# Kernel tuning notes

Hardware: AMD Instinct MI355X
Metric: run time of the kernel (lower is better)

The kernel has to match this reference:

```python
import jax, jax.numpy as jnp
import numpy as np

N_MODES = 4
N_STAGES = 7
CTRL_HIDDEN = 128
PASS_DIM = 32
MAX_PASSES = 12


def _ln(x, g, b, eps=1e-5):
    m = x.mean(-1, keepdims=True)
    v = ((x - m) ** 2).mean(-1, keepdims=True)
    return (x - m) * jax.lax.rsqrt(v + eps) * g + b


def setup_inputs() -> dict:
    B, T, D, H = 8, 2048, 768, 256
    ks = jax.random.split(jax.random.key(0), 16)
    n = lambda i, shp, s=0.02: (jax.random.normal(ks[i], shp) * s).astype(jnp.float32)
    inp = {
        'h': jax.random.normal(ks[0], (B, T, D), jnp.float32),
        'emb_x': jax.random.normal(ks[1], (B, T, D), jnp.float32),
        'lam': jax.random.uniform(ks[2], (B, T, D), jnp.float32, 0.1, 2.0),
        'mu_prev': jax.random.normal(ks[3], (B, T, D), jnp.float32),
        'base_w1': n(4, (H, D)), 'base_b1': jnp.zeros((H,), jnp.float32),
        'base_w2': n(5, (N_STAGES * N_STAGES, H)), 'base_b2': jnp.zeros((N_STAGES * N_STAGES,), jnp.float32),
        'ln_g': jnp.ones((D,), jnp.float32), 'ln_b': jnp.zeros((D,), jnp.float32),
        'mlp_w1': n(6, (CTRL_HIDDEN, 2 * D + 4)), 'mlp_b1': jnp.zeros((CTRL_HIDDEN,), jnp.float32),
        'mlp_w2': n(7, (CTRL_HIDDEN, CTRL_HIDDEN)), 'mlp_b2': jnp.zeros((CTRL_HIDDEN,), jnp.float32),
        'pass_embed': n(8, (MAX_PASSES, PASS_DIM)),
        'ch_w': n(9, (N_MODES, CTRL_HIDDEN), 0.01), 'ch_b': jnp.zeros((N_MODES,), jnp.float32),
        'ph_w': n(10, (N_MODES, PASS_DIM), 0.01), 'ph_b': jnp.zeros((N_MODES,), jnp.float32),
        'bil_w': n(11, (PASS_DIM * N_MODES, CTRL_HIDDEN), 0.01),
        'mode_bias': jnp.zeros((N_MODES,), jnp.float32),
        'ms_w': n(12, (N_STAGES, N_MODES), 0.01),
    }
    # STAGE_GRAPH: banded stage transition mask (self + next stage + reset-to-0)
    sg = np.zeros((N_STAGES, N_STAGES), np.int32)
    for i in range(N_STAGES):
        sg[i, i] = 1
        sg[i, (i + 1) % N_STAGES] = 1
        sg[i, 0] = 1
    inp['stage_graph'] = jnp.asarray(sg)
    inp['pass_idx'] = 3
    return inp


def reference(h, emb_x, lam, mu_prev, base_w1, base_b1, base_w2, base_b2,
              ln_g, ln_b, mlp_w1, mlp_b1, mlp_w2, mlp_b2, pass_embed,
              ch_w, ch_b, ph_w, ph_b, bil_w, mode_bias, ms_w,
              stage_graph, pass_idx):
    B, T, D = h.shape
    # base transition MLP: (B,T,D) -> (B,T,7,7)
    base = (jax.nn.silu(h @ base_w1.T + base_b1) @ base_w2.T + base_b2).reshape(B, T, N_STAGES, N_STAGES)
    # TokenwiseController
    mu_normed = _ln(h, ln_g, ln_b)
    log_lam = jnp.log(jnp.maximum(lam, 1e-6))
    mean_ll = log_lam.mean(-1, keepdims=True)
    std_ll = jnp.maximum(jnp.std(log_lam, axis=-1, ddof=1, keepdims=True), 1e-6)
    dmu = jnp.sqrt(((h - mu_prev) ** 2).mean(-1, keepdims=True) + 1e-8)
    pf = jnp.full((B, T, 1), pass_idx / max(MAX_PASSES - 1, 1), h.dtype)
    r = jnp.concatenate([mu_normed, jax.lax.stop_gradient(emb_x), mean_ll, std_ll, dmu, pf], -1)
    c = jax.nn.silu(r @ mlp_w1.T + mlp_b1) @ mlp_w2.T + mlp_b2  # (B,T,128)
    u = pass_embed[pass_idx]  # (32,)
    content_logits = c @ ch_w.T + ch_b          # (B,T,4)
    pass_logits = u @ ph_w.T + ph_b             # (4,)
    bil = (c @ bil_w.T).reshape(B, T, N_MODES, PASS_DIM)
    bilinear_logits = jnp.einsum('btmk,k->btm', bil, u)
    ell = content_logits + pass_logits + bilinear_logits + mode_bias
    alpha = jax.nn.softmax(ell, axis=-1)        # (B,T,4)
    stage_bias = alpha @ ms_w.T                 # (B,T,7)
    # masked stage-graph softmax
    raw = base + stage_bias[:, :, None, :]
    raw = jnp.where(stage_graph[None, None] == 0, -jnp.inf, raw)
    K = jax.nn.softmax(raw, axis=-1)            # (B,T,7,7)
    return K, alpha
```

## Files before the change

### kernel.cpp

```cpp
#include <hip/hip_runtime.h>
#include <hip/hip_bf16.h>
#include <cstdint>
#include <cstddef>

#define NT      16384
#define DIM     768
#define TT      16
#define ALPHA_OFF 802816

#define WS_WFHI   0
#define WS_WFLO   196608
#define WS_GA     393216
#define WS_CBIAS  393344
#define WS_V1     393472
#define WS_V2     393600
#define WS_V3     393728
#define WS_CHEFF  393856
#define WS_C4     394368

typedef __attribute__((ext_vector_type(8))) short short8;
typedef __attribute__((ext_vector_type(4))) float f32x4;

__device__ __forceinline__ float silu_f(float x) { return x / (1.0f + expf(-x)); }

__device__ __forceinline__ unsigned short f2bf_u(float x) {
    union { __hip_bfloat16 b; unsigned short u; } c;
    c.b = __float2bfloat16(x);
    return c.u;
}
__device__ __forceinline__ float bf2f_u(unsigned short u) {
    union { unsigned short u; __hip_bfloat16 b; } c;
    c.u = u;
    return __bfloat162float(c.b);
}

__global__ void k_prep(const float* __restrict__ bw1, const float* __restrict__ mw1,
                       const float* __restrict__ g, const float* __restrict__ mb1,
                       const float* __restrict__ lnb, const float* __restrict__ pe,
                       const float* __restrict__ chw, const float* __restrict__ chb,
                       const float* __restrict__ phw, const float* __restrict__ phb,
                       const float* __restrict__ bil, const float* __restrict__ mob,
                       const int* __restrict__ pidxp, unsigned int* __restrict__ wfh,
                       unsigned int* __restrict__ wfl,
                       float* __restrict__ gA, float* __restrict__ cbias,
                       float* __restrict__ v1, float* __restrict__ v2,
                       float* __restrict__ v3, float* __restrict__ cheff_t,
                       float* __restrict__ c4) {
    __shared__ float tilebuf[64][65];
    __shared__ float u[32];
    int tid = threadIdx.x;

    if (blockIdx.x == 96) {
        int pidx = *pidxp;
        if (tid < 32) u[tid] = pe[pidx * 32 + tid];
        __syncthreads();
        {
            int j = tid >> 1, half = tid & 1;
            const float* row = mw1 + (size_t)j * 1540 + half * 384;
            const float* gp = g + half * 384;
            const float* bp = lnb + half * 384;
            float sg_ = 0.f, sb_ = 0.f;
            for (int k = 0; k < 384; k += 4) {
                float4 rv = *(const float4*)(row + k);
                float4 gv = *(const float4*)(gp + k);
                float4 bv = *(const float4*)(bp + k);
                sg_ += rv.x * gv.x + rv.y * gv.y + rv.z * gv.z + rv.w * gv.w;
                sb_ += rv.x * bv.x + rv.y * bv.y + rv.z * bv.z + rv.w * bv.w;
            }
            sg_ += __shfl_xor(sg_, 1);
            sb_ += __shfl_xor(sb_, 1);
            if (half == 0) {
                const float* rowf = mw1 + (size_t)j * 1540;
                float pf = (float)pidx * (1.0f / 11.0f);
                gA[j] = sg_;
                v1[j] = rowf[1536];
                v2[j] = rowf[1537];
                v3[j] = rowf[1538];
                cbias[j] = sb_ + pf * rowf[1539] + mb1[j];
            }
        }
        for (int idx = tid; idx < 512; idx += 256) {
            int k = idx >> 2, m = idx & 3;
            float s = chw[m * 128 + k];
            for (int kk = 0; kk < 32; kk++) s += u[kk] * bil[(size_t)(m * 32 + kk) * 128 + k];
            cheff_t[k * 4 + m] = s;
        }
        if (tid < 4) {
            float s = chb[tid] + phb[tid] + mob[tid];
            for (int kk = 0; kk < 32; kk++) s += u[kk] * phw[tid * 32 + kk];
            c4[tid] = s;
        }
        return;
    }

    int jt = blockIdx.x & 7, kt = blockIdx.x >> 3;
    int j0 = jt * 64, k0 = kt * 64;

    {
        int jl = tid >> 2, kc = (tid & 3) * 16;
        int j = j0 + jl;
        const float* src;
        if (j0 < 256)      src = bw1 + (size_t)j * DIM + k0;
        else if (j0 < 384) src = mw1 + (size_t)(j - 256) * 1540 + k0;
        else               src = mw1 + (size_t)(j - 384) * 1540 + 768 + k0;
#pragma unroll
        for (int q = 0; q < 16; q += 4) {
            float4 v = *(const float4*)(src + kc + q);
            tilebuf[jl][kc + q + 0] = v.x;
            tilebuf[jl][kc + q + 1] = v.y;
            tilebuf[jl][kc + q + 2] = v.z;
            tilebuf[jl][kc + q + 3] = v.w;
        }
    }
    __syncthreads();
    {
        int l = tid & 63, item = tid >> 6;
        int ks_loc = item & 1, tp = item >> 1;
#pragma unroll
        for (int it = 0; it < 2; ++it) {
            int tile_loc = tp * 2 + it;
            int tile = jt * 4 + tile_loc;
            int ks = kt * 2 + ks_loc;
            int jl = tile_loc * 16 + (l & 15);
            int klb = ks_loc * 32 + (l >> 4) * 8;
            bool applyg = (tile >= 16 && tile < 24);
            unsigned int hiw[4], low[4];
#pragma unroll
            for (int p = 0; p < 4; ++p) {
                float x0 = tilebuf[jl][klb + 2 * p];
                float x1 = tilebuf[jl][klb + 2 * p + 1];
                if (applyg) {
                    x0 *= g[k0 + klb + 2 * p];
                    x1 *= g[k0 + klb + 2 * p + 1];
                }
                unsigned short h0 = f2bf_u(x0), h1 = f2bf_u(x1);
                unsigned short l0 = f2bf_u(x0 - bf2f_u(h0));
                unsigned short l1 = f2bf_u(x1 - bf2f_u(h1));
                hiw[p] = (unsigned int)h0 | ((unsigned int)h1 << 16);
                low[p] = (unsigned int)l0 | ((unsigned int)l1 << 16);
            }
            size_t idx = (size_t)(ks * 32 + tile) * 64 + l;
            ((uint4*)wfh)[idx] = make_uint4(hiw[0], hiw[1], hiw[2], hiw[3]);
            ((uint4*)wfl)[idx] = make_uint4(low[0], low[1], low[2], low[3]);
        }
    }
}

__device__ __forceinline__ void stage_ld2(const float* __restrict__ h,
                                          const float* __restrict__ ex,
                                          int tok0, int kb, int tid,
                                          float4& o0, float4& o1) {
    int row = tid >> 3, seg = tid & 7;
    const float* src = (row < 16) ? (h + (size_t)(tok0 + row) * DIM)
                                  : (ex + (size_t)(tok0 + row - 16) * DIM);
    o0 = *(const float4*)(src + kb + seg * 8);
    o1 = *(const float4*)(src + kb + seg * 8 + 4);
}
__device__ __forceinline__ void stage_st2(float* buf, int tid, float4 v0, float4 v1) {
    int row = tid >> 3, seg = tid & 7;
    float* d = buf + row * 68 + seg * 8;
    *(float4*)(d) = v0;
    *(float4*)(d + 4) = v1;
}

__launch_bounds__(256, 4)
__global__ void k_main(const float* __restrict__ h, const float* __restrict__ ex,
                       const float* __restrict__ lam, const float* __restrict__ mup,
                       const float* __restrict__ bb1, const float* __restrict__ bw2,
                       const float* __restrict__ bb2, const float* __restrict__ mw2,
                       const float* __restrict__ mb2, const float* __restrict__ msw,
                       const int* __restrict__ sg, const unsigned int* __restrict__ wfh,
                       const unsigned int* __restrict__ wfl,
                       const float* __restrict__ gA, const float* __restrict__ cbias,
                       const float* __restrict__ v1w, const float* __restrict__ v2w,
                       const float* __restrict__ v3w, const float* __restrict__ cheff_t,
                       const float* __restrict__ c4, float* __restrict__ out) {
    __shared__ float F[8036];
    float* c1      = F + 4352;
    float* basebuf = F + 6464;
    float* stats   = F + 7248;
    float* cheff_s = F + 7376;
    float* alpha_s = F + 7888;
    float* c4_s    = F + 7952;
    float* msw_s   = F + 7956;
    int*   sg_s    = (int*)(F + 7984);

    const int tid = threadIdx.x;
    const int bid = blockIdx.x;
    const int tok0 = bid * TT;

    if (tid < 49) sg_s[tid] = sg[tid];
    if (tid >= 64 && tid < 92) msw_s[tid - 64] = msw[tid - 64];
    if (tid >= 96 && tid < 100) c4_s[tid - 96] = c4[tid - 96];
    for (int i = tid; i < 512; i += 256) cheff_s[i] = cheff_t[i];

    float4 p0, p1;
    stage_ld2(h, ex, tok0, 0, tid, p0, p1);

    {
        int t = tid >> 4, r = tid & 15;
        const float* hp = h + (size_t)(tok0 + t) * DIM;
        const float* lp = lam + (size_t)(tok0 + t) * DIM;
        const float* mp = mup + (size_t)(tok0 + t) * DIM;
        float sh = 0.f, sh2 = 0.f, sll = 0.f, sll2 = 0.f, sd = 0.f;
        for (int i = 0; i < 12; i++) {
            int k0 = i * 64 + r * 4;
            float4 hv = *(const float4*)(hp + k0);
            float4 lv = *(const float4*)(lp + k0);
            float4 mv = *(const float4*)(mp + k0);
#pragma unroll
            for (int e = 0; e < 4; e++) {
                float hx = (&hv.x)[e];
                float lx = fmaxf((&lv.x)[e], 1e-6f);
                float mx = (&mv.x)[e];
                sh += hx; sh2 += hx * hx;
                float ll = logf(lx);
                sll += ll; sll2 += ll * ll;
                float dd = hx - mx; sd += dd * dd;
            }
        }
#pragma unroll
        for (int off = 1; off < 16; off <<= 1) {
            sh += __shfl_xor(sh, off);  sh2 += __shfl_xor(sh2, off);
            sll += __shfl_xor(sll, off); sll2 += __shfl_xor(sll2, off);
            sd += __shfl_xor(sd, off);
        }
        if (r == 0) {
            float m = sh * (1.f / 768.f);
            float var = sh2 * (1.f / 768.f) - m * m;
            float istd = rsqrtf(var + 1e-5f);
            float mll = sll * (1.f / 768.f);
            float vll = (sll2 - 768.f * mll * mll) * (1.f / 767.f);
            float sstd = fmaxf(sqrtf(fmaxf(vll, 0.f)), 1e-6f);
            float dmu = sqrtf(sd * (1.f / 768.f) + 1e-8f);
            float* st = stats + t * 8;
            st[0] = m; st[1] = istd; st[2] = mll; st[3] = sstd; st[4] = dmu;
        }
    }

    stage_st2(F, tid, p0, p1);
    __syncthreads();

    const int w = tid >> 6, l = tid & 63;
    const int arowbase = (l & 15) + ((w == 3) ? 16 : 0);
    const int mrow0 = (l >> 4) * 4;
    const int q8 = (l >> 4) * 8;

    f32x4 acc[8];
#pragma unroll
    for (int t = 0; t < 8; ++t) acc[t] = (f32x4){0.f, 0.f, 0.f, 0.f};

    const short8* wph = (const short8*)wfh + (size_t)(8 * w) * 64 + l;
    const short8* wpl = (const short8*)wfl + (size_t)(8 * w) * 64 + l;

    int cur = 0;
    for (int c = 0; c < 12; ++c) {
        const bool more = (c + 1 < 12);
        const float* ab = F + cur * 2176;
        float* nb = F + (cur ^ 1) * 2176;
        if (more) stage_ld2(h, ex, tok0, (c + 1) * 64, tid, p0, p1);
#pragma unroll
        for (int ks_loc = 0; ks_loc < 2; ++ks_loc) {
            const int ks = c * 2 + ks_loc;
            const float* ar = ab + arowbase * 68 + ks_loc * 32 + q8;
            float4 a0  = *(const float4*)(ar);
            float4 a1v = *(const float4*)(ar + 4);
            float av[8] = {a0.x, a0.y, a0.z, a0.w, a1v.x, a1v.y, a1v.z, a1v.w};
            short8 Ah, Al;
#pragma unroll
            for (int j = 0; j < 8; ++j) {
                unsigned short hb = f2bf_u(av[j]);
                Ah[j] = (short)hb;
                Al[j] = (short)f2bf_u(av[j] - bf2f_u(hb));
            }
            const short8* bh = wph + (size_t)ks * 2048;
            const short8* bl = wpl + (size_t)ks * 2048;
#pragma unroll
            for (int t = 0; t < 8; ++t) {
                short8 Bh = bh[t * 64];
                short8 Bl = bl[t * 64];
                acc[t] = __builtin_amdgcn_mfma_f32_16x16x32_bf16(Ah, Bh, acc[t], 0, 0, 0);
                acc[t] = __builtin_amdgcn_mfma_f32_16x16x32_bf16(Ah, Bl, acc[t], 0, 0, 0);
                acc[t] = __builtin_amdgcn_mfma_f32_16x16x32_bf16(Al, Bh, acc[t], 0, 0, 0);
            }
        }
        if (more) stage_st2(nb, tid, p0, p1);
        __syncthreads();
        cur ^= 1;
    }

    float* a1 = F;
    if (w < 2) {
#pragma unroll
        for (int t = 0; t < 8; ++t) {
            int j = (8 * w + t) * 16 + (l & 15);
            float b = bb1[j];
#pragma unroll
            for (int r = 0; r < 4; ++r)
                a1[(mrow0 + r) * 260 + j] = silu_f(acc[t][r] + b);
        }
    } else if (w == 2) {
#pragma unroll
        for (int t = 0; t < 8; ++t) {
            int jj = t * 16 + (l & 15);
            float ga = gA[jj], cb = cbias[jj];
            float w1 = v1w[jj], w2 = v2w[jj], w3 = v3w[jj];
#pragma unroll
            for (int r = 0; r < 4; ++r) {
                const float* st = stats + (mrow0 + r) * 8;
                c1[(mrow0 + r) * 132 + jj] =
                    st[1] * acc[t][r] - st[1] * st[0] * ga + st[2] * w1 + st[3] * w2 +
                    st[4] * w3 + cb;
            }
        }
    }
    __syncthreads();
    if (w == 3) {
#pragma unroll
        for (int t = 0; t < 8; ++t) {
            int jj = t * 16 + (l & 15);
#pragma unroll
            for (int r = 0; r < 4; ++r) {
                float* cp = &c1[(mrow0 + r) * 132 + jj];
                *cp = silu_f(*cp + acc[t][r]);
            }
        }
    }
    __syncthreads();

    for (int o = tid; o < TT * 49; o += 256) {
        int t = o / 49, s = o - t * 49;
        const float* ar = a1 + t * 260;
        const float* wr = bw2 + s * 256;
        float accv = bb2[s];
        for (int k = 0; k < 256; k += 4) {
            float4 av = *(const float4*)(ar + k);
            float4 wv = *(const float4*)(wr + k);
            accv += av.x * wv.x + av.y * wv.y + av.z * wv.z + av.w * wv.w;
        }
        basebuf[o] = accv;
    }
    __syncthreads();

    float* cbuf = F;
    {
        int j = tid & 127, tg = tid >> 7;
        float accv[8];
#pragma unroll
        for (int tt = 0; tt < 8; tt++) accv[tt] = 0.f;
        const float* wr = mw2 + (size_t)j * 128;
        const float* cr = c1 + tg * 8 * 132;
        for (int k = 0; k < 128; k += 4) {
            float4 wv = *(const float4*)(wr + k);
#pragma unroll
            for (int tt = 0; tt < 8; tt++) {
                float4 cv = *(const float4*)(cr + tt * 132 + k);
                accv[tt] += cv.x * wv.x + cv.y * wv.y + cv.z * wv.z + cv.w * wv.w;
            }
        }
        float b = mb2[j];
        __syncthreads();
#pragma unroll
        for (int tt = 0; tt < 8; tt++) cbuf[(tg * 8 + tt) * 132 + j] = accv[tt] + b;
    }
    __syncthreads();

    if (tid < 64) {
        int t = tid >> 2, m = tid & 3;
        const float* cr = cbuf + t * 132;
        float e = c4_s[m];
        for (int k = 0; k < 128; k++) e += cr[k] * cheff_s[k * 4 + m];
        float mx = fmaxf(e, __shfl_xor(e, 1));
        mx = fmaxf(mx, __shfl_xor(mx, 2));
        float ev = expf(e - mx);
        float sum = ev + __shfl_xor(ev, 1);
        sum += __shfl_xor(sum, 2);
        float al = ev / sum;
        alpha_s[t * 4 + m] = al;
        out[ALPHA_OFF + (size_t)(tok0 + t) * 4 + m] = al;
    }
    __syncthreads();

    if (tid < TT * 7) {
        int t = tid / 7, i = tid - t * 7;
        const float* al = alpha_s + t * 4;
        float sb[7];
#pragma unroll
        for (int s = 0; s < 7; s++)
            sb[s] = al[0] * msw_s[s * 4 + 0] + al[1] * msw_s[s * 4 + 1] +
                    al[2] * msw_s[s * 4 + 2] + al[3] * msw_s[s * 4 + 3];
        const float* br = basebuf + t * 49 + i * 7;
        const int* mrow = sg_s + i * 7;
        float vals[7];
        float mx = -1e30f;
#pragma unroll
        for (int j = 0; j < 7; j++) {
            float vv = br[j] + sb[j];
            vals[j] = mrow[j] ? vv : -1e30f;
            mx = fmaxf(mx, vals[j]);
        }
        float e[7], sum = 0.f;
#pragma unroll
        for (int j = 0; j < 7; j++) {
            e[j] = mrow[j] ? expf(vals[j] - mx) : 0.f;
            sum += e[j];
        }
        float inv = 1.f / sum;
        size_t off = (size_t)(tok0 + t) * 49 + i * 7;
#pragma unroll
        for (int j = 0; j < 7; j++) out[off + j] = e[j] * inv;
    }
}

extern "C" void kernel_launch(void* const* d_in, const int* in_sizes, int n_in,
                              void* d_out, int out_size, void* d_ws, size_t ws_size,
                              hipStream_t stream) {
    const float* h    = (const float*)d_in[0];
    const float* ex   = (const float*)d_in[1];
    const float* lam  = (const float*)d_in[2];
    const float* mup  = (const float*)d_in[3];
    const float* bw1  = (const float*)d_in[4];
    const float* bb1  = (const float*)d_in[5];
    const float* bw2  = (const float*)d_in[6];
    const float* bb2  = (const float*)d_in[7];
    const float* lng  = (const float*)d_in[8];
    const float* lnb  = (const float*)d_in[9];
    const float* mw1  = (const float*)d_in[10];
    const float* mb1  = (const float*)d_in[11];
    const float* mw2  = (const float*)d_in[12];
    const float* mb2  = (const float*)d_in[13];
    const float* pe   = (const float*)d_in[14];
    const float* chw  = (const float*)d_in[15];
    const float* chb  = (const float*)d_in[16];
    const float* phw  = (const float*)d_in[17];
    const float* phb  = (const float*)d_in[18];
    const float* bil  = (const float*)d_in[19];
    const float* mob  = (const float*)d_in[20];
    const float* msw  = (const float*)d_in[21];
    const int*   sg   = (const int*)d_in[22];
    const int*   pidx = (const int*)d_in[23];
    float* out = (float*)d_out;
    float* ws = (float*)d_ws;

    unsigned int* wfh = (unsigned int*)(ws + WS_WFHI);
    unsigned int* wfl = (unsigned int*)(ws + WS_WFLO);
    float* gA    = ws + WS_GA;
    float* cbias = ws + WS_CBIAS;
    float* v1    = ws + WS_V1;
    float* v2    = ws + WS_V2;
    float* v3    = ws + WS_V3;
    float* cheff = ws + WS_CHEFF;
    float* c4    = ws + WS_C4;

    hipLaunchKernelGGL(k_prep, dim3(97), dim3(256), 0, stream, bw1, mw1, lng, mb1, lnb, pe,
                       chw, chb, phw, phb, bil, mob, pidx, wfh, wfl, gA, cbias, v1, v2, v3,
                       cheff, c4);
    hipLaunchKernelGGL(k_main, dim3(NT / TT), dim3(256), 0, stream, h, ex, lam, mup, bb1, bw2,
                       bb2, mw2, mb2, msw, sg, wfh, wfl, gA, cbias, v1, v2, v3, cheff, c4, out);
}
```

Measured before the change: 432.4 us.

## Process 32 tokens per block to reuse weight fragments across two M tiles

```diff
diff --git a/kernel.cpp b/kernel.cpp
--- a/kernel.cpp
+++ b/kernel.cpp
@@ -5,7 +5,7 @@
 
 #define NT      16384
 #define DIM     768
-#define TT      16
+#define TT      32
 #define ALPHA_OFF 802816
 
 #define WS_WFHI   0
@@ -146,24 +146,28 @@
     }
 }
 
-__device__ __forceinline__ void stage_ld2(const float* __restrict__ h,
+__device__ __forceinline__ void stage_ld4(const float* __restrict__ h,
                                           const float* __restrict__ ex,
-                                          int tok0, int kb, int tid,
-                                          float4& o0, float4& o1) {
-    int row = tid >> 3, seg = tid & 7;
-    const float* src = (row < 16) ? (h + (size_t)(tok0 + row) * DIM)
-                                  : (ex + (size_t)(tok0 + row - 16) * DIM);
-    o0 = *(const float4*)(src + kb + seg * 8);
-    o1 = *(const float4*)(src + kb + seg * 8 + 4);
-}
-__device__ __forceinline__ void stage_st2(float* buf, int tid, float4 v0, float4 v1) {
-    int row = tid >> 3, seg = tid & 7;
-    float* d = buf + row * 68 + seg * 8;
-    *(float4*)(d) = v0;
-    *(float4*)(d + 4) = v1;
-}
-
-__launch_bounds__(256, 4)
+                                          int tok0, int kb, int tid, float4 o[4]) {
+    int row = tid >> 2, seg = tid & 3;
+    const float* src = (row < 32) ? (h + (size_t)(tok0 + row) * DIM)
+                                  : (ex + (size_t)(tok0 + row - 32) * DIM);
+    const float* p = src + kb + seg * 16;
+    o[0] = *(const float4*)(p);
+    o[1] = *(const float4*)(p + 4);
+    o[2] = *(const float4*)(p + 8);
+    o[3] = *(const float4*)(p + 12);
+}
+__device__ __forceinline__ void stage_st4(float* buf, int tid, const float4 o[4]) {
+    int row = tid >> 2, seg = tid & 3;
+    float* d = buf + row * 68 + seg * 16;
+    *(float4*)(d) = o[0];
+    *(float4*)(d + 4) = o[1];
+    *(float4*)(d + 8) = o[2];
+    *(float4*)(d + 12) = o[3];
+}
+
+__launch_bounds__(256, 2)
 __global__ void k_main(const float* __restrict__ h, const float* __restrict__ ex,
                        const float* __restrict__ lam, const float* __restrict__ mup,
                        const float* __restrict__ bb1, const float* __restrict__ bw2,
@@ -175,15 +179,15 @@
                        const float* __restrict__ v1w, const float* __restrict__ v2w,
                        const float* __restrict__ v3w, const float* __restrict__ cheff_t,
                        const float* __restrict__ c4, float* __restrict__ out) {
-    __shared__ float F[8036];
-    float* c1      = F + 4352;
-    float* basebuf = F + 6464;
-    float* stats   = F + 7248;
-    float* cheff_s = F + 7376;
-    float* alpha_s = F + 7888;
-    float* c4_s    = F + 7952;
-    float* msw_s   = F + 7956;
-    int*   sg_s    = (int*)(F + 7984);
+    __shared__ float F[15473];
+    float* c1      = F + 8704;
+    float* basebuf = F + 12928;
+    float* stats   = F + 14496;
+    float* cheff_s = F + 14752;
+    float* alpha_s = F + 15264;
+    float* c4_s    = F + 15392;
+    float* msw_s   = F + 15396;
+    int*   sg_s    = (int*)(F + 15424);
 
     const int tid = threadIdx.x;
     const int bid = blockIdx.x;
@@ -194,17 +198,17 @@
     if (tid >= 96 && tid < 100) c4_s[tid - 96] = c4[tid - 96];
     for (int i = tid; i < 512; i += 256) cheff_s[i] = cheff_t[i];
 
-    float4 p0, p1;
-    stage_ld2(h, ex, tok0, 0, tid, p0, p1);
+    float4 p[4];
+    stage_ld4(h, ex, tok0, 0, tid, p);
 
     {
-        int t = tid >> 4, r = tid & 15;
+        int t = tid >> 3, r = tid & 7;
         const float* hp = h + (size_t)(tok0 + t) * DIM;
         const float* lp = lam + (size_t)(tok0 + t) * DIM;
         const float* mp = mup + (size_t)(tok0 + t) * DIM;
         float sh = 0.f, sh2 = 0.f, sll = 0.f, sll2 = 0.f, sd = 0.f;
-        for (int i = 0; i < 12; i++) {
-            int k0 = i * 64 + r * 4;
+        for (int i = 0; i < 24; i++) {
+            int k0 = i * 32 + r * 4;
             float4 hv = *(const float4*)(hp + k0);
             float4 lv = *(const float4*)(lp + k0);
             float4 mv = *(const float4*)(mp + k0);
@@ -220,7 +224,7 @@
             }
         }
 #pragma unroll
-        for (int off = 1; off < 16; off <<= 1) {
+        for (int off = 1; off < 8; off <<= 1) {
             sh += __shfl_xor(sh, off);  sh2 += __shfl_xor(sh2, off);
             sll += __shfl_xor(sll, off); sll2 += __shfl_xor(sll2, off);
             sd += __shfl_xor(sd, off);
@@ -238,17 +242,19 @@
         }
     }
 
-    stage_st2(F, tid, p0, p1);
+    stage_st4(F, tid, p);
     __syncthreads();
 
     const int w = tid >> 6, l = tid & 63;
-    const int arowbase = (l & 15) + ((w == 3) ? 16 : 0);
-    const int mrow0 = (l >> 4) * 4;
-    const int q8 = (l >> 4) * 8;
-
-    f32x4 acc[8];
-#pragma unroll
-    for (int t = 0; t < 8; ++t) acc[t] = (f32x4){0.f, 0.f, 0.f, 0.f};
+    const int lm = l & 15, lk = l >> 4;
+    const int abase = ((w == 3) ? 32 : 0) + lm;
+    const int q8 = lk * 8;
+
+    f32x4 acc[2][8];
+#pragma unroll
+    for (int m = 0; m < 2; ++m)
+#pragma unroll
+        for (int t = 0; t < 8; ++t) acc[m][t] = (f32x4){0.f, 0.f, 0.f, 0.f};
 
     const short8* wph = (const short8*)wfh + (size_t)(8 * w) * 64 + l;
     const short8* wpl = (const short8*)wfl + (size_t)(8 * w) * 64 + l;
@@ -256,35 +262,49 @@
     int cur = 0;
     for (int c = 0; c < 12; ++c) {
         const bool more = (c + 1 < 12);
-        const float* ab = F + cur * 2176;
-        float* nb = F + (cur ^ 1) * 2176;
-        if (more) stage_ld2(h, ex, tok0, (c + 1) * 64, tid, p0, p1);
+        const float* ab = F + cur * 4352;
+        float* nb = F + (cur ^ 1) * 4352;
+        if (more) stage_ld4(h, ex, tok0, (c + 1) * 64, tid, p);
 #pragma unroll
         for (int ks_loc = 0; ks_loc < 2; ++ks_loc) {
             const int ks = c * 2 + ks_loc;
-            const float* ar = ab + arowbase * 68 + ks_loc * 32 + q8;
-            float4 a0  = *(const float4*)(ar);
-            float4 a1v = *(const float4*)(ar + 4);
-            float av[8] = {a0.x, a0.y, a0.z, a0.w, a1v.x, a1v.y, a1v.z, a1v.w};
-            short8 Ah, Al;
-#pragma unroll
-            for (int j = 0; j < 8; ++j) {
-                unsigned short hb = f2bf_u(av[j]);
-                Ah[j] = (short)hb;
-                Al[j] = (short)f2bf_u(av[j] - bf2f_u(hb));
-            }
             const short8* bh = wph + (size_t)ks * 2048;
             const short8* bl = wpl + (size_t)ks * 2048;
+            short8 BH[8], BL[8];
 #pragma unroll
             for (int t = 0; t < 8; ++t) {
-                short8 Bh = bh[t * 64];
-                short8 Bl = bl[t * 64];
-                acc[t] = __builtin_amdgcn_mfma_f32_16x16x32_bf16(Ah, Bh, acc[t], 0, 0, 0);
-                acc[t] = __builtin_amdgcn_mfma_f32_16x16x32_bf16(Ah, Bl, acc[t], 0, 0, 0);
-                acc[t] = __builtin_amdgcn_mfma_f32_16x16x32_bf16(Al, Bh, acc[t], 0, 0, 0);
-            }
-        }
-        if (more) stage_st2(nb, tid, p0, p1);
+                BH[t] = bh[t * 64];
+                BL[t] = bl[t * 64];
+            }
+            const float* ar0 = ab + abase * 68 + ks_loc * 32 + q8;
+            const float* ar1 = ar0 + 16 * 68;
+            float4 a00 = *(const float4*)(ar0);
+            float4 a01 = *(const float4*)(ar0 + 4);
+            float4 a10 = *(const float4*)(ar1);
+            float4 a11 = *(const float4*)(ar1 + 4);
+            float av0[8] = {a00.x, a00.y, a00.z, a00.w, a01.x, a01.y, a01.z, a01.w};
+            float av1[8] = {a10.x, a10.y, a10.z, a10.w, a11.x, a11.y, a11.z, a11.w};
+            short8 Ah0, Al0, Ah1, Al1;
+#pragma unroll
+            for (int j = 0; j < 8; ++j) {
+                unsigned short hb0 = f2bf_u(av0[j]);
+                Ah0[j] = (short)hb0;
+                Al0[j] = (short)f2bf_u(av0[j] - bf2f_u(hb0));
+                unsigned short hb1 = f2bf_u(av1[j]);
+                Ah1[j] = (short)hb1;
+                Al1[j] = (short)f2bf_u(av1[j] - bf2f_u(hb1));
+            }
+#pragma unroll
+            for (int t = 0; t < 8; ++t) {
+                acc[0][t] = __builtin_amdgcn_mfma_f32_16x16x32_bf16(Ah0, BH[t], acc[0][t], 0, 0, 0);
+                acc[1][t] = __builtin_amdgcn_mfma_f32_16x16x32_bf16(Ah1, BH[t], acc[1][t], 0, 0, 0);
+                acc[0][t] = __builtin_amdgcn_mfma_f32_16x16x32_bf16(Ah0, BL[t], acc[0][t], 0, 0, 0);
+                acc[1][t] = __builtin_amdgcn_mfma_f32_16x16x32_bf16(Ah1, BL[t], acc[1][t], 0, 0, 0);
+                acc[0][t] = __builtin_amdgcn_mfma_f32_16x16x32_bf16(Al0, BH[t], acc[0][t], 0, 0, 0);
+                acc[1][t] = __builtin_amdgcn_mfma_f32_16x16x32_bf16(Al1, BH[t], acc[1][t], 0, 0, 0);
+            }
+        }
+        if (more) stage_st4(nb, tid, p);
         __syncthreads();
         cur ^= 1;
     }
@@ -293,37 +313,45 @@
     if (w < 2) {
 #pragma unroll
         for (int t = 0; t < 8; ++t) {
-            int j = (8 * w + t) * 16 + (l & 15);
+            int j = (8 * w + t) * 16 + lm;
             float b = bb1[j];
 #pragma unroll
-            for (int r = 0; r < 4; ++r)
-                a1[(mrow0 + r) * 260 + j] = silu_f(acc[t][r] + b);
+            for (int m = 0; m < 2; ++m)
+#pragma unroll
+                for (int r = 0; r < 4; ++r)
+                    a1[(m * 16 + lk * 4 + r) * 260 + j] = silu_f(acc[m][t][r] + b);
         }
     } else if (w == 2) {
 #pragma unroll
         for (int t = 0; t < 8; ++t) {
-            int jj = t * 16 + (l & 15);
+            int jj = t * 16 + lm;
             float ga = gA[jj], cb = cbias[jj];
             float w1 = v1w[jj], w2 = v2w[jj], w3 = v3w[jj];
 #pragma unroll
-            for (int r = 0; r < 4; ++r) {
-                const float* st = stats + (mrow0 + r) * 8;
-                c1[(mrow0 + r) * 132 + jj] =
-                    st[1] * acc[t][r] - st[1] * st[0] * ga + st[2] * w1 + st[3] * w2 +
-                    st[4] * w3 + cb;
-            }
+            for (int m = 0; m < 2; ++m)
+#pragma unroll
+                for (int r = 0; r < 4; ++r) {
+                    int tok = m * 16 + lk * 4 + r;
+                    const float* st = stats + tok * 8;
+                    c1[tok * 132 + jj] =
+                        st[1] * acc[m][t][r] - st[1] * st[0] * ga + st[2] * w1 +
+                        st[3] * w2 + st[4] * w3 + cb;
+                }
         }
     }
     __syncthreads();
     if (w == 3) {
 #pragma unroll
         for (int t = 0; t < 8; ++t) {
-            int jj = t * 16 + (l & 15);
-#pragma unroll
-            for (int r = 0; r < 4; ++r) {
-                float* cp = &c1[(mrow0 + r) * 132 + jj];
-                *cp = silu_f(*cp + acc[t][r]);
-            }
+            int jj = t * 16 + lm;
+#pragma unroll
+            for (int m = 0; m < 2; ++m)
+#pragma unroll
+                for (int r = 0; r < 4; ++r) {
+                    int tok = m * 16 + lk * 4 + r;
+                    float* cp = &c1[tok * 132 + jj];
+                    *cp = silu_f(*cp + acc[m][t][r]);
+                }
         }
     }
     __syncthreads();
@@ -345,15 +373,15 @@
     float* cbuf = F;
     {
         int j = tid & 127, tg = tid >> 7;
-        float accv[8];
-#pragma unroll
-        for (int tt = 0; tt < 8; tt++) accv[tt] = 0.f;
+        float accv[16];
+#pragma unroll
+        for (int tt = 0; tt < 16; tt++) accv[tt] = 0.f;
         const float* wr = mw2 + (size_t)j * 128;
-        const float* cr = c1 + tg * 8 * 132;
+        const float* cr = c1 + tg * 16 * 132;
         for (int k = 0; k < 128; k += 4) {
             float4 wv = *(const float4*)(wr + k);
 #pragma unroll
-            for (int tt = 0; tt < 8; tt++) {
+            for (int tt = 0; tt < 16; tt++) {
                 float4 cv = *(const float4*)(cr + tt * 132 + k);
                 accv[tt] += cv.x * wv.x + cv.y * wv.y + cv.z * wv.z + cv.w * wv.w;
             }
@@ -361,11 +389,11 @@
         float b = mb2[j];
         __syncthreads();
 #pragma unroll
-        for (int tt = 0; tt < 8; tt++) cbuf[(tg * 8 + tt) * 132 + j] = accv[tt] + b;
-    }
-    __syncthreads();
-
-    if (tid < 64) {
+        for (int tt = 0; tt < 16; tt++) cbuf[(tg * 16 + tt) * 132 + j] = accv[tt] + b;
+    }
+    __syncthreads();
+
+    if (tid < 128) {
         int t = tid >> 2, m = tid & 3;
         const float* cr = cbuf + t * 132;
         float e = c4_s[m];
```

Result: faster. 411.2 us (-4.9%).
